# Kernel optimization log

Hardware: AMD Instinct MI355X
Metric: run time of the kernel (lower is better)

## Reference

```python
import jax, jax.numpy as jnp
import numpy as np

MOLS = 64
ATOMS = 256
N = MOLS * ATOMS
K_GB = 32
K_GNN = 16
HID = 128
OFFSET = 0.009            # GB dielectric offset (nm)
ALPHA, BETA, GAMMA = 1.0, 0.8, 4.85  # OBC2 coefficients
EPS_FACTOR = 138.935456   # Coulomb constant, kJ*nm/(mol*e^2)
PREF = -EPS_FACTOR * (1.0 - 1.0 / 78.5)


def _edges(key, k_neigh):
    # random intra-molecule neighbors, no self loops (mimics radius-graph structure)
    src = jnp.repeat(jnp.arange(N), k_neigh)
    off = jax.random.randint(key, (N * k_neigh,), 1, ATOMS)
    dst = (src // ATOMS) * ATOMS + (src % ATOMS + off) % ATOMS
    return jnp.stack([src, dst]).astype(jnp.int32)


def setup_inputs() -> dict:
    key = jax.random.key(0)
    ks = jax.random.split(key, 8)
    pos = (jax.random.uniform(ks[0], (N, 3), jnp.float32) * 1.5)
    q = jax.random.uniform(ks[1], (N, 1), jnp.float32) - 0.5
    rad = 0.15 + 0.05 * jax.random.uniform(ks[2], (N, 1), jnp.float32)
    scl = 0.8 + 0.2 * jax.random.uniform(ks[3], (N, 1), jnp.float32)
    rest = jax.random.uniform(ks[4], (N, 4), jnp.float32)
    atom_features = jnp.concatenate([q, rad, scl, rest], axis=1)
    batch = jnp.repeat(jnp.arange(MOLS), ATOMS).astype(jnp.int32)
    edge_index = _edges(ks[5], K_GB)
    gnn_edge_index = _edges(ks[6], K_GNN)

    def lin(k, fi, fo):
        return (jax.random.normal(k, (fi, fo), jnp.float32) / np.float32(np.sqrt(fi)),
                jnp.zeros((fo,), jnp.float32))
    kw = jax.random.split(ks[7], 6)
    i1_w1, i1_b1 = lin(kw[0], 2 * 2 + 1, HID)
    i1_w2, i1_b2 = lin(kw[1], HID, HID)
    i2_w1, i2_b1 = lin(kw[2], 2 * HID + 1, HID)
    i2_w2, i2_b2 = lin(kw[3], HID, HID)
    i3_w1, i3_b1 = lin(kw[4], 2 * HID + 1, HID)
    i3_w2, i3_b2 = lin(kw[5], HID, 1)
    return dict(pos=pos, atom_features=atom_features, batch=batch,
                edge_index=edge_index, gnn_edge_index=gnn_edge_index,
                i1_w1=i1_w1, i1_b1=i1_b1, i1_w2=i1_w2, i1_b2=i1_b2,
                i2_w1=i2_w1, i2_b1=i2_b1, i2_w2=i2_w2, i2_b2=i2_b2,
                i3_w1=i3_w1, i3_b1=i3_b1, i3_w2=i3_w2, i3_b2=i3_b2)


def _dist(pos, ei):
    d2 = jnp.sum((pos[ei[0]] - pos[ei[1]]) ** 2, axis=1)
    return jnp.sqrt(d2 + 1e-12)


def _gb_energies(pos, feats, ei):
    # GBNeck_interaction (Born radii via HCT descreening integral, OBC2 rescale)
    # followed by GBNeck_energies (pairwise GB + self energy), per-atom [N,1]
    n = pos.shape[0]
    src, dst = ei[0], ei[1]
    d = _dist(pos, ei)
    q, radius, scale = feats[:, 0], feats[:, 1], feats[:, 2]
    rho = radius - OFFSET
    sr_j = (scale * rho)[src]
    rho_i = rho[dst]
    U = d + sr_j
    L = jnp.maximum(rho_i, jnp.abs(d - sr_j))
    I = 0.5 * (1.0 / L - 1.0 / U
               + 0.25 * (d - sr_j ** 2 / d) * (1.0 / U ** 2 - 1.0 / L ** 2)
               + 0.5 * jnp.log(L / U) / d)
    I = jnp.where(rho_i < U, I, 0.0)
    Isum = jax.ops.segment_sum(I, dst, num_segments=n)
    psi = Isum * rho
    B = 1.0 / (1.0 / rho - jnp.tanh(ALPHA * psi - BETA * psi ** 2 + GAMMA * psi ** 3) / radius)
    Bi, Bj = B[dst], B[src]
    f_gb = jnp.sqrt(d ** 2 + Bi * Bj * jnp.exp(-d ** 2 / (4.0 * Bi * Bj)))
    e_pair = 0.5 * PREF * q[dst] * q[src] / f_gb  # 0.5: edges are double counted
    e = 0.5 * PREF * q ** 2 / B + jax.ops.segment_sum(e_pair, dst, num_segments=n)
    return e[:, None]


def _in_layer(x, ei, d, w1, b1, w2, b2):
    # IN_layer_all_swish_2pass: edge MLP on [x_i || x_j || d] + scatter-add
    n = x.shape[0]
    m = jnp.concatenate([x[ei[0]], x[ei[1]], d[:, None]], axis=1)
    h = jax.nn.silu(m @ w1 + b1)
    return jax.ops.segment_sum(h @ w2 + b2, ei[1], num_segments=n)


def _energies_all(pos, feats, ei, gei,
                  i1_w1, i1_b1, i1_w2, i1_b2,
                  i2_w1, i2_b1, i2_w2, i2_b2,
                  i3_w1, i3_b1, i3_w2, i3_b2):
    e_gb = _gb_energies(pos, feats, ei)
    d_gnn = _dist(pos, gei)
    x = jax.nn.silu(_in_layer(feats[:, :2], gei, d_gnn, i1_w1, i1_b1, i1_w2, i1_b2))
    x = jax.nn.silu(_in_layer(x, gei, d_gnn, i2_w1, i2_b1, i2_w2, i2_b2))
    x = _in_layer(x, gei, d_gnn, i3_w1, i3_b1, i3_w2, i3_b2)
    return e_gb + x


def reference(pos, atom_features, batch, edge_index, gnn_edge_index,
              i1_w1, i1_b1, i1_w2, i1_b2,
              i2_w1, i2_b1, i2_w2, i2_b2,
              i3_w1, i3_b1, i3_w2, i3_b2):
    ws = (i1_w1, i1_b1, i1_w2, i1_b2, i2_w1, i2_b1, i2_w2, i2_b2,
          i3_w1, i3_b1, i3_w2, i3_b2)
    efun = lambda p: _energies_all(p, atom_features, edge_index, gnn_edge_index, *ws)
    energies, vjp = jax.vjp(efun, pos)  # [N,1]
    (gpos,) = vjp(jnp.ones_like(energies))
    forces = -gpos
    energy = jax.ops.segment_sum(energies[:, 0], batch, num_segments=MOLS)[:, None]
    return energy, forces
```

## Files before the change

### kernel.cpp

```cpp
#include <hip/hip_runtime.h>
#include <hip/hip_bf16.h>

#define NATOMS 16384
#define MOLS   64
#define ATOMSM 256
#define EGB    524288
#define EGNN   262144
#define HID    128
#define NH     (NATOMS*HID)

#define OFFSETC 0.009f
#define ALPHAC  1.0f
#define BETAC   0.8f
#define GAMMAC  4.85f
#define PREFC   (-138.935456f*(1.0f-1.0f/78.5f))

typedef __hip_bfloat16 bf;
typedef __attribute__((ext_vector_type(8))) short bf8v;
typedef __attribute__((ext_vector_type(4))) float f4v;
typedef unsigned int uint;

__device__ __forceinline__ float b2f(bf x){ return __bfloat162float(x); }
__device__ __forceinline__ bf f2b(float x){ return __float2bfloat16(x); }
__device__ __forceinline__ short f2s(float x){ bf h = f2b(x); return *(short*)&h; }
__device__ __forceinline__ float s2f(short s){
    unsigned int x = ((unsigned int)(unsigned short)s) << 16;
    return __uint_as_float(x);
}
__device__ __forceinline__ float frcp(float x){ return __builtin_amdgcn_rcpf(x); }
__device__ __forceinline__ float frsq(float x){ return __builtin_amdgcn_rsqf(x); }
__device__ __forceinline__ float fsqrt(float x){ return __builtin_amdgcn_sqrtf(x); }
__device__ __forceinline__ float sigf(float x){ return frcp(1.0f+__expf(-x)); }
__device__ __forceinline__ float waveRed(float v){
    v += __shfl_xor(v,32); v += __shfl_xor(v,16); v += __shfl_xor(v,8);
    v += __shfl_xor(v,4);  v += __shfl_xor(v,2);  v += __shfl_xor(v,1);
    return v;
}
__device__ __forceinline__ uint pack2(float a, float b){
    return (uint)(unsigned short)f2s(a) | ((uint)(unsigned short)f2s(b) << 16);
}
__device__ __forceinline__ float lo2f(uint w){ return __uint_as_float(w << 16); }
__device__ __forceinline__ float hi2f(uint w){ return __uint_as_float(w & 0xffff0000u); }

__device__ __forceinline__ float red16(float (&A)[16], int lane){
#pragma unroll
    for (int i=0;i<8;i++){
        float send = (lane & 16) ? A[i] : A[i+8];
        float recv = __shfl_xor(send, 16);
        A[i] = ((lane & 16) ? A[i+8] : A[i]) + recv;
    }
#pragma unroll
    for (int i=0;i<4;i++){
        float send = (lane & 8) ? A[i] : A[i+4];
        float recv = __shfl_xor(send, 8);
        A[i] = ((lane & 8) ? A[i+4] : A[i]) + recv;
    }
#pragma unroll
    for (int i=0;i<2;i++){
        float send = (lane & 4) ? A[i] : A[i+2];
        float recv = __shfl_xor(send, 4);
        A[i] = ((lane & 4) ? A[i+2] : A[i]) + recv;
    }
    {
        float send = (lane & 2) ? A[0] : A[1];
        float recv = __shfl_xor(send, 2);
        A[0] = ((lane & 2) ? A[1] : A[0]) + recv;
    }
    A[0] += __shfl_xor(A[0], 32);
    A[0] += __shfl_xor(A[0], 1);
    return A[0];
}

__global__ __launch_bounds__(256) void k_A(
    const float* __restrict__ A2, const float* __restrict__ C1,
    const float* __restrict__ A3, const float* __restrict__ C2,
    short* __restrict__ C1t, short* __restrict__ C2t,
    short* __restrict__ A2at, short* __restrict__ A2bt,
    short* __restrict__ A3at, short* __restrict__ A3bt,
    short* __restrict__ rA2a, short* __restrict__ rA2b,
    short* __restrict__ rA3a, short* __restrict__ rA3b,
    short* __restrict__ rC1, short* __restrict__ rC2,
    const float* __restrict__ feat, const float* __restrict__ A1,
    bf* __restrict__ u1, bf* __restrict__ v1,
    const float* __restrict__ pos, const int* __restrict__ ei,
    float* __restrict__ Isum,
    const int* __restrict__ gei, float* __restrict__ dgnn, int* __restrict__ cnt)
{
    int tid = threadIdx.x;
    if (blockIdx.x < 64){
        int gid = blockIdx.x*256 + tid;
        int j = gid >> 7, k = gid & 127;
        C1t[gid]  = f2s(C1[k*HID+j]);
        C2t[gid]  = f2s(C2[k*HID+j]);
        A2at[gid] = f2s(A2[k*HID+j]);
        A2bt[gid] = f2s(A2[(HID+k)*HID+j]);
        A3at[gid] = f2s(A3[k*HID+j]);
        A3bt[gid] = f2s(A3[(HID+k)*HID+j]);
        rA2a[gid] = f2s(A2[gid]);
        rA2b[gid] = f2s(A2[HID*HID+gid]);
        rA3a[gid] = f2s(A3[gid]);
        rA3b[gid] = f2s(A3[HID*HID+gid]);
        rC1[gid]  = f2s(C1[gid]);
        rC2[gid]  = f2s(C2[gid]);
    } else if (blockIdx.x < 4160){
        int gid2 = (blockIdx.x-64)*256 + tid;
        int i = gid2 >> 6, k2 = (gid2 & 63)*2;
        float q = feat[7*i+0], r = feat[7*i+1];
        float u0 = q*A1[k2]         + r*A1[HID+k2];
        float u1v= q*A1[k2+1]       + r*A1[HID+k2+1];
        float v0 = q*A1[2*HID+k2]   + r*A1[3*HID+k2];
        float v1v= q*A1[2*HID+k2+1] + r*A1[3*HID+k2+1];
        ushort2 uu, vv;
        uu.x = (unsigned short)f2s(u0); uu.y = (unsigned short)f2s(u1v);
        vv.x = (unsigned short)f2s(v0); vv.y = (unsigned short)f2s(v1v);
        *(ushort2*)((short*)u1 + (size_t)i*HID + k2) = uu;
        *(ushort2*)((short*)v1 + (size_t)i*HID + k2) = vv;
    } else if (blockIdx.x < 4672){
        __shared__ float sPx[256], sPy[256], sPz[256], sRho[256], sSr[256];
        __shared__ float sI[256];
        int bb = blockIdx.x - 4160;
        int mbase = (bb >> 3) * 256;
        {
            int i = mbase + tid;
            sPx[tid]=pos[3*i]; sPy[tid]=pos[3*i+1]; sPz[tid]=pos[3*i+2];
            float rad = feat[7*i+1], sc = feat[7*i+2];
            float rho = rad - OFFSETC;
            sRho[tid]=rho; sSr[tid]=sc*rho;
            sI[tid]=0.f;
        }
        __syncthreads();
        int T = bb*256 + tid;
        int s = T >> 3, p = T & 7;
        int sl = s & 255;
        int e0 = s*32 + p*4;
        float px = sPx[sl], py = sPy[sl], pz = sPz[sl];
        float sr = sSr[sl];
        float srr = sr*sr;
        const int* dP = ei + EGB;
        int4 d4 = *(const int4*)(dP + e0);
        int dls[4] = {d4.x&255, d4.y&255, d4.z&255, d4.w&255};
#pragma unroll
        for (int j=0;j<4;j++){
            int dl = dls[j];
            float dx = px - sPx[dl];
            float dy = py - sPy[dl];
            float dz = pz - sPz[dl];
            float d2 = dx*dx+dy*dy+dz*dz + 1e-12f;
            float rd = frsq(d2);
            float d  = d2*rd;
            float rho_i = sRho[dl];
            float U = d + sr;
            if (rho_i < U){
                float L = fmaxf(rho_i, fabsf(d - sr));
                float invU = frcp(U), invL = frcp(L);
                float I = 0.5f*invL - 0.5f*invU
                        + 0.125f*(d - srr*rd)*(invU*invU - invL*invL)
                        + 0.25f*__logf(L*invU)*rd;
                atomicAdd(&sI[dl], I);
            }
        }
        __syncthreads();
        atomicAdd(&Isum[mbase + tid], sI[tid]);
    } else {
        int e = (blockIdx.x-4672)*256 + tid;
        int s = gei[e], dd = gei[EGNN+e];
        float dx = pos[3*s+0] - pos[3*dd+0];
        float dy = pos[3*s+1] - pos[3*dd+1];
        float dz = pos[3*s+2] - pos[3*dd+2];
        dgnn[e] = fsqrt(dx*dx+dy*dy+dz*dz + 1e-12f);
        atomicAdd(&cnt[dd], 1);
    }
}

__global__ __launch_bounds__(256) void k_B(
    const float* __restrict__ feat, const float* __restrict__ Isum,
    float* __restrict__ Bv, float* __restrict__ cB, float* __restrict__ gB,
    float* __restrict__ egb,
    const int* __restrict__ cnt, int* __restrict__ rptr,
    const int* __restrict__ gei, const float* __restrict__ dgnn,
    int* __restrict__ csr, int2* __restrict__ csr2)
{
    int t = threadIdx.x;
    if (blockIdx.x < 64){
        int i = blockIdx.x*256 + t;
        float q   = feat[7*i+0];
        float rad = feat[7*i+1];
        float rho = rad - OFFSETC;
        float psi = Isum[i]*rho;
        float u = psi*(ALPHAC + psi*(-BETAC + GAMMAC*psi));
        float tt = tanhf(u);
        float rrad = frcp(rad);
        float B = frcp(frcp(rho) - tt*rrad);
        Bv[i] = B;
        float du = ALPHAC + psi*(-2.0f*BETAC + 3.0f*GAMMAC*psi);
        cB[i] = B*B*((1.0f-tt*tt)*rrad)*du*rho;
        float Cs = 0.5f*PREFC*q*q;
        float rB = frcp(B);
        egb[i] = Cs*rB;
        gB[i]  = -Cs*rB*rB;
    } else {
        __shared__ int sc[256];
        __shared__ int lcur[256];
        int m = blockIdx.x - 64;
        int c = cnt[m*256+t];
        sc[t] = c; __syncthreads();
        for (int off=1; off<256; off<<=1){
            int x = (t>=off) ? sc[t-off] : 0;
            __syncthreads();
            sc[t] += x;
            __syncthreads();
        }
        int exl = sc[t] - c;
        rptr[m*256+t] = m*4096 + exl;
        lcur[t] = exl;
        __syncthreads();
        int e0 = m*4096;
        for (int j=t; j<4096; j+=256){
            int e = e0 + j;
            int dl = gei[EGNN+e] & 255;
            float d = dgnn[e];
            int p = atomicAdd(&lcur[dl], 1);
            int idx = e0 + p;
            csr[idx] = e;
            int2 rec; rec.x = (e >> 4) << 8;
            rec.y = __float_as_int(d);
            csr2[idx] = rec;
        }
    }
}

template<bool WSDS>
__device__ __forceinline__ void edge_fwd_wave(
    int dst, int lane,
    const int2* __restrict__ csr2, const int* __restrict__ rptr, const int* __restrict__ cnt,
    const uint* __restrict__ u, const uint* __restrict__ v,
    const float* __restrict__ wdp, const float* __restrict__ bb,
    uint* __restrict__ Hs, uint* __restrict__ Sds)
{
    int n = cnt[dst], r0 = rptr[dst];
    float2 wd = *(const float2*)&wdp[2*lane];
    float2 b2 = *(const float2*)&bb[2*lane];
    uint vp = v[dst*64 + lane];
    float base0 = lo2f(vp) + b2.x;
    float base1 = hi2f(vp) + b2.y;
    float h0=0.f,h1=0.f,e0a=0.f,e1a=0.f;
    for (int j0=0; j0<n; j0+=64){
        int m = n - j0; if (m > 64) m = 64;
        int rx = 0, ry = 0;
        if (lane < m){ int2 rc = csr2[r0+j0+lane]; rx = rc.x; ry = rc.y; }
#pragma unroll 8
        for (int j=0;j<m;j++){
            uint off = (uint)__builtin_amdgcn_readlane(rx, j);
            float d  = __uint_as_float((unsigned)__builtin_amdgcn_readlane(ry, j));
            const uint* urow = (const uint*)((const char*)u + off);
            uint up = urow[lane];
            float a0 = fmaf(d, wd.x, base0 + lo2f(up));
            float a1 = fmaf(d, wd.y, base1 + hi2f(up));
            float s0 = sigf(a0), s1 = sigf(a1);
            float p0 = a0*s0, p1 = a1*s1;
            h0 += p0; h1 += p1;
            if (WSDS){
                e0a = fmaf(s0, 1.f + a0 - p0, e0a);
                e1a = fmaf(s1, 1.f + a1 - p1, e1a);
            }
        }
    }
    Hs[dst*64+lane] = pack2(h0,h1);
    if (WSDS) Sds[dst*64+lane] = pack2(e0a,e1a);
}

__global__ __launch_bounds__(256,8) void k_ef0C(
    const float* __restrict__ pos, const float* __restrict__ feat,
    const int* __restrict__ ei, const float* __restrict__ Bv,
    float* __restrict__ egb, float* __restrict__ gdgb, float* __restrict__ gB,
    const int2* __restrict__ csr2, const int* __restrict__ rptr, const int* __restrict__ cnt,
    const uint* __restrict__ u, const uint* __restrict__ v,
    const float* __restrict__ wdp, const float* __restrict__ bb,
    uint* __restrict__ Hs)
{
    int tid = threadIdx.x;
    if (blockIdx.x < 512){
        __shared__ float sPx[256], sPy[256], sPz[256], sB[256], sQf[256];
        __shared__ float sE[256], sG[256];
        int mbase = (blockIdx.x >> 3) * 256;
        {
            int i = mbase + tid;
            sPx[tid]=pos[3*i]; sPy[tid]=pos[3*i+1]; sPz[tid]=pos[3*i+2];
            sB[tid]=Bv[i]; sQf[tid]=feat[7*i+0];
            sE[tid]=0.f; sG[tid]=0.f;
        }
        __syncthreads();
        int T = blockIdx.x*256 + tid;
        int s = T >> 3, p = T & 7;
        int sl = s & 255;
        int e0 = s*32 + p*4;
        float px = sPx[sl], py = sPy[sl], pz = sPz[sl];
        float qs = sQf[sl];
        float Bs = sB[sl];
        float gsrc = 0.f;
        const int* dP = ei + EGB;
        int4 d4 = *(const int4*)(dP + e0);
        int dls[4] = {d4.x&255, d4.y&255, d4.z&255, d4.w&255};
#pragma unroll
        for (int j=0;j<4;j++){
            int dl = dls[j];
            float dx = px - sPx[dl];
            float dy = py - sPy[dl];
            float dz = pz - sPz[dl];
            float d2 = dx*dx+dy*dy+dz*dz + 1e-12f;
            float d  = d2*frsq(d2);
            float Bd = sB[dl];
            float C = 0.5f*PREFC*sQf[dl]*qs;
            float P = Bd*Bs;
            float qq = 0.25f*d2*frcp(P);
            float ex = __expf(-qq);
            float f2 = d2 + P*ex;
            float rf = frsq(f2);
            float f3i = rf*rf*rf;
            gdgb[e0+j] = -C*d*(1.f - 0.25f*ex)*f3i;
            float common = -C*ex*(1.f + qq)*0.5f*f3i;
            atomicAdd(&sE[dl], C*rf);
            atomicAdd(&sG[dl], common*Bs);
            gsrc += common*Bd;
        }
        gsrc += __shfl_xor(gsrc,1);
        gsrc += __shfl_xor(gsrc,2);
        gsrc += __shfl_xor(gsrc,4);
        if (p==0) atomicAdd(&sG[sl], gsrc);
        __syncthreads();
        atomicAdd(&egb[mbase + tid], sE[tid]);
        atomicAdd(&gB[mbase + tid],  sG[tid]);
    } else {
        int lane = tid & 63, wid = tid >> 6;
        int dst = (blockIdx.x-512)*4 + wid;
        edge_fwd_wave<false>(dst, lane, csr2, rptr, cnt, u, v, wdp, bb, Hs, nullptr);
    }
}

__global__ __launch_bounds__(256,8) void k_ef1E(
    const float* __restrict__ pos, const float* __restrict__ feat,
    const int* __restrict__ ei, const float* __restrict__ cB,
    const float* __restrict__ gB,
    const float* __restrict__ gdgb, float* __restrict__ grad,
    const int2* __restrict__ csr2, const int* __restrict__ rptr, const int* __restrict__ cnt,
    const uint* __restrict__ u, const uint* __restrict__ v,
    const float* __restrict__ wdp, const float* __restrict__ bb,
    uint* __restrict__ Hs, uint* __restrict__ Sds)
{
    int tid = threadIdx.x;
    if (blockIdx.x < 512){
        __shared__ float sPx[256], sPy[256], sPz[256], sRho[256], sSr[256], sCg[256];
        __shared__ float sGx[256], sGy[256], sGz[256];
        int mbase = (blockIdx.x >> 3) * 256;
        {
            int i = mbase + tid;
            sPx[tid]=pos[3*i]; sPy[tid]=pos[3*i+1]; sPz[tid]=pos[3*i+2];
            float rad = feat[7*i+1], sc = feat[7*i+2];
            float rho = rad - OFFSETC;
            sRho[tid]=rho; sSr[tid]=sc*rho;
            sCg[tid]=cB[i]*gB[i];
            sGx[tid]=0.f; sGy[tid]=0.f; sGz[tid]=0.f;
        }
        __syncthreads();
        int T = blockIdx.x*256 + tid;
        int s = T >> 3, p = T & 7;
        int sl = s & 255;
        int e0 = s*32 + p*4;
        float px = sPx[sl], py = sPy[sl], pz = sPz[sl];
        float sr = sSr[sl];
        float srr = sr*sr;
        float gx=0.f, gy=0.f, gz=0.f;
        const int* dP = ei + EGB;
        int4 d4 = *(const int4*)(dP + e0);
        int dls[4] = {d4.x&255, d4.y&255, d4.z&255, d4.w&255};
#pragma unroll
        for (int j=0;j<4;j++){
            int dl = dls[j];
            float dx = px - sPx[dl];
            float dy = py - sPy[dl];
            float dz = pz - sPz[dl];
            float d2 = dx*dx+dy*dy+dz*dz + 1e-12f;
            float rd = frsq(d2);
            float d  = d2*rd;
            float rd2 = rd*rd;
            float rho_i = sRho[dl];
            float U = d + sr;
            float gd = gdgb[e0+j];
            if (rho_i < U){
                float aa = fabsf(d - sr);
                float L, Lp;
                if (rho_i >= aa){ L = rho_i; Lp = 0.f; }
                else { L = aa; Lp = (d >= sr) ? 1.f : -1.f; }
                float invU = frcp(U), invL = frcp(L);
                float invU2=invU*invU, invL2=invL*invL;
                float dIdd = -0.5f*Lp*invL2 + 0.5f*invU2
                    + 0.125f*(1.f + srr*rd2)*(invU2 - invL2)
                    + 0.125f*(d - srr*rd)*(2.f*Lp*invL2*invL - 2.f*invU2*invU)
                    + 0.25f*((Lp*invL - invU)*rd - __logf(L*invU)*rd2);
                gd += sCg[dl]*dIdd;
            }
            float c = gd*rd;
            gx += c*dx; gy += c*dy; gz += c*dz;
            atomicAdd(&sGx[dl], -c*dx);
            atomicAdd(&sGy[dl], -c*dy);
            atomicAdd(&sGz[dl], -c*dz);
        }
        gx += __shfl_xor(gx,1); gx += __shfl_xor(gx,2); gx += __shfl_xor(gx,4);
        gy += __shfl_xor(gy,1); gy += __shfl_xor(gy,2); gy += __shfl_xor(gy,4);
        gz += __shfl_xor(gz,1); gz += __shfl_xor(gz,2); gz += __shfl_xor(gz,4);
        if (p==0){
            atomicAdd(&sGx[sl], gx);
            atomicAdd(&sGy[sl], gy);
            atomicAdd(&sGz[sl], gz);
        }
        __syncthreads();
        int i = mbase + tid;
        atomicAdd(&grad[3*i+0], sGx[tid]);
        atomicAdd(&grad[3*i+1], sGy[tid]);
        atomicAdd(&grad[3*i+2], sGz[tid]);
    } else {
        int lane = tid & 63, wid = tid >> 6;
        int dst = (blockIdx.x-512)*4 + wid;
        edge_fwd_wave<true>(dst, lane, csr2, rptr, cnt, u, v, wdp, bb, Hs, Sds);
    }
}

__global__ __launch_bounds__(256) void k_node_fwd_uv_mfma(
    const short* __restrict__ Hs, const int* __restrict__ cnt,
    const short* __restrict__ Ct, const float* __restrict__ D,
    const short* __restrict__ Aat, const short* __restrict__ Abt,
    bf* __restrict__ dsz, bf* __restrict__ u, bf* __restrict__ v)
{
    __shared__ short sx[64*HID];
    int tid = threadIdx.x;
    int lane = tid & 63, w = tid >> 6;
    int m0 = blockIdx.x*64 + w*16;
    int ar = lane & 15, kg = lane >> 4;
    bf8v af[4];
#pragma unroll
    for (int s=0;s<4;s++) af[s] = *(const bf8v*)&Hs[(size_t)(m0+ar)*HID + s*32 + kg*8];
    f4v acc[8];
#pragma unroll
    for (int nt=0;nt<8;nt++){
        acc[nt] = (f4v){0.f,0.f,0.f,0.f};
        const short* bp = Ct + (nt*16+ar)*HID + kg*8;
#pragma unroll
        for (int s=0;s<4;s++){
            bf8v bv = *(const bf8v*)(bp + s*32);
            acc[nt] = __builtin_amdgcn_mfma_f32_16x16x32_bf16(af[s], bv, acc[nt], 0,0,0);
        }
    }
    float cn[4];
#pragma unroll
    for (int r=0;r<4;r++) cn[r] = (float)cnt[m0 + kg*4 + r];
#pragma unroll
    for (int nt=0;nt<8;nt++){
        int j = nt*16 + ar;
        float Dj = D[j];
#pragma unroll
        for (int r=0;r<4;r++){
            int m = m0 + kg*4 + r;
            float zv = acc[nt][r] + cn[r]*Dj;
            float sg = sigf(zv);
            dsz[(size_t)m*HID + j] = f2b(sg*(1.f + zv*(1.f - sg)));
            sx[(w*16 + kg*4 + r)*HID + j] = f2s(zv*sg);
        }
    }
    __syncthreads();
#pragma unroll
    for (int s=0;s<4;s++) af[s] = *(const bf8v*)&sx[(w*16+ar)*HID + s*32 + kg*8];
    f4v au[8], av[8];
#pragma unroll
    for (int nt=0;nt<8;nt++){
        au[nt] = (f4v){0.f,0.f,0.f,0.f};
        av[nt] = (f4v){0.f,0.f,0.f,0.f};
        const short* bpa = Aat + (nt*16+ar)*HID + kg*8;
        const short* bpb = Abt + (nt*16+ar)*HID + kg*8;
#pragma unroll
        for (int s=0;s<4;s++){
            bf8v ba = *(const bf8v*)(bpa + s*32);
            bf8v bb = *(const bf8v*)(bpb + s*32);
            au[nt] = __builtin_amdgcn_mfma_f32_16x16x32_bf16(af[s], ba, au[nt], 0,0,0);
            av[nt] = __builtin_amdgcn_mfma_f32_16x16x32_bf16(af[s], bb, av[nt], 0,0,0);
        }
    }
#pragma unroll
    for (int nt=0;nt<8;nt++){
        int j = nt*16 + ar;
#pragma unroll
        for (int r=0;r<4;r++){
            int m = m0 + kg*4 + r;
            u[(size_t)m*HID + j] = f2b(au[nt][r]);
            v[(size_t)m*HID + j] = f2b(av[nt][r]);
        }
    }
}

__global__ __launch_bounds__(256,6) void k_l3(
    const int2* __restrict__ csr2, const int* __restrict__ rptr, const int* __restrict__ cnt,
    const int* __restrict__ gei, const float* __restrict__ dgnn,
    const uint* __restrict__ u, const uint* __restrict__ v,
    const float* __restrict__ A3, const float* __restrict__ B3,
    const float* __restrict__ C3, const float* __restrict__ D3,
    uint* __restrict__ Gd, float* __restrict__ x3,
    uint* __restrict__ Gs, float* __restrict__ gdg)
{
    int lane = threadIdx.x & 63, wid = threadIdx.x >> 6;
    const float* wdp = A3 + 256*HID;
    if (blockIdx.x < NATOMS/4){
        int dst = blockIdx.x*4 + wid;
        int n = cnt[dst], r0 = rptr[dst];
        float2 wd = *(const float2*)&wdp[2*lane];
        float2 b2 = *(const float2*)&B3[2*lane];
        float2 ck = *(const float2*)&C3[2*lane];
        uint vp = v[dst*64 + lane];
        float base0 = lo2f(vp) + b2.x;
        float base1 = hi2f(vp) + b2.y;
        float h0=0.f,h1=0.f,e0a=0.f,e1a=0.f;
        for (int j0=0; j0<n; j0+=64){
            int m = n - j0; if (m > 64) m = 64;
            int rx = 0, ry = 0;
            if (lane < m){ int2 rc = csr2[r0+j0+lane]; rx = rc.x; ry = rc.y; }
#pragma unroll 8
            for (int j=0;j<m;j++){
                uint off = (uint)__builtin_amdgcn_readlane(rx, j);
                float d  = __uint_as_float((unsigned)__builtin_amdgcn_readlane(ry, j));
                const uint* urow = (const uint*)((const char*)u + off);
                uint up = urow[lane];
                float a0 = fmaf(d, wd.x, base0 + lo2f(up));
                float a1 = fmaf(d, wd.y, base1 + hi2f(up));
                float s0 = sigf(a0), s1 = sigf(a1);
                float p0 = a0*s0, p1 = a1*s1;
                h0 += p0; h1 += p1;
                e0a = fmaf(s0, 1.f + a0 - p0, e0a);
                e1a = fmaf(s1, 1.f + a1 - p1, e1a);
            }
        }
        Gd[dst*64+lane] = pack2(ck.x*e0a, ck.y*e1a);
        float px = waveRed(ck.x*h0 + ck.y*h1);
        if (lane==0) x3[dst] = px + (float)n*D3[0];
    } else {
        int s = (blockIdx.x - NATOMS/4)*4 + wid;
        int doff = 0, dbit = 0;
        if (lane < 16){
            doff = gei[EGNN + s*16 + lane] << 8;
            dbit = __float_as_int(dgnn[s*16+lane]);
        }
        float2 wd = *(const float2*)&wdp[2*lane];
        float2 b2 = *(const float2*)&B3[2*lane];
        float2 ck = *(const float2*)&C3[2*lane];
        uint up = u[s*64 + lane];
        float us0 = lo2f(up) + b2.x;
        float us1 = hi2f(up) + b2.y;
        float cw0 = ck.x*wd.x, cw1 = ck.y*wd.y;
        float gs0=0.f, gs1=0.f;
        float A[16];
#pragma unroll
        for (int t=0;t<16;t++){
            uint off = (uint)__builtin_amdgcn_readlane(doff, t);
            float d = __uint_as_float((unsigned)__builtin_amdgcn_readlane(dbit, t));
            const uint* vrow = (const uint*)((const char*)v + off);
            uint vp = vrow[lane];
            float a0 = fmaf(d, wd.x, us0 + lo2f(vp));
            float a1 = fmaf(d, wd.y, us1 + hi2f(vp));
            float s0 = sigf(a0), s1 = sigf(a1);
            float p0 = a0*s0, p1 = a1*s1;
            float dv0 = s0*(1.f + a0 - p0);
            float dv1 = s1*(1.f + a1 - p1);
            gs0 += dv0; gs1 += dv1;
            A[t] = fmaf(dv1, cw1, dv0*cw0);
        }
        Gs[s*64+lane] = pack2(ck.x*gs0, ck.y*gs1);
        float tot = red16(A, lane);
        if (lane < 32 && !(lane & 1)) gdg[s*16 + (lane>>1)] = tot;
    }
}

__global__ __launch_bounds__(256,6) void k_bwd_src(
    const int* __restrict__ gei, const float* __restrict__ dgnn,
    const uint* __restrict__ u, const uint* __restrict__ v,
    const float* __restrict__ wdp, const float* __restrict__ bb,
    const uint* __restrict__ gH,
    uint* __restrict__ Gs, float* __restrict__ gdg)
{
    int lane = threadIdx.x & 63, wid = threadIdx.x >> 6;
    int s = blockIdx.x*4 + wid;
    int doff = 0, dbit = 0;
    if (lane < 16){
        doff = gei[EGNN + s*16 + lane] << 8;
        dbit = __float_as_int(dgnn[s*16+lane]);
    }
    float gold = gdg[s*16 + ((lane>>1)&15)];
    float2 wd = *(const float2*)&wdp[2*lane];
    float2 b2 = *(const float2*)&bb[2*lane];
    uint up = u[s*64 + lane];
    float us0 = lo2f(up) + b2.x;
    float us1 = hi2f(up) + b2.y;
    float gs0=0.f, gs1=0.f;
    float A[16];
#pragma unroll
    for (int t=0;t<16;t++){
        uint off = (uint)__builtin_amdgcn_readlane(doff, t);
        float d = __uint_as_float((unsigned)__builtin_amdgcn_readlane(dbit, t));
        const uint* vrow = (const uint*)((const char*)v + off);
        const uint* grow = (const uint*)((const char*)gH + off);
        uint vp = vrow[lane];
        uint gp = grow[lane];
        float a0 = fmaf(d, wd.x, us0 + lo2f(vp));
        float a1 = fmaf(d, wd.y, us1 + hi2f(vp));
        float s0 = sigf(a0), s1 = sigf(a1);
        float p0 = a0*s0, p1 = a1*s1;
        float ga0 = s0*(1.f + a0 - p0) * lo2f(gp);
        float ga1 = s1*(1.f + a1 - p1) * hi2f(gp);
        gs0 += ga0; gs1 += ga1;
        A[t] = fmaf(ga1, wd.y, ga0*wd.x);
    }
    if (Gs) Gs[s*64+lane] = pack2(gs0, gs1);
    float tot = red16(A, lane);
    if (lane < 32 && !(lane & 1)) gdg[s*16 + (lane>>1)] = gold + tot;
}

__global__ __launch_bounds__(256) void k_gx_node_bwd_mfma(
    const short* __restrict__ Gs, const short* __restrict__ Gd,
    const short* __restrict__ gHin, const short* __restrict__ Sds,
    const short* __restrict__ Ra, const short* __restrict__ Rb,
    const bf* __restrict__ dsz, const short* __restrict__ Rc,
    bf* __restrict__ gHout)
{
    __shared__ short st[64*HID];
    int lane = threadIdx.x & 63, w = threadIdx.x >> 6;
    int m0 = blockIdx.x*64 + w*16;
    int ar = lane & 15, kg = lane >> 4;
    bf8v as_[4], ad_[4];
#pragma unroll
    for (int s=0;s<4;s++)
        as_[s] = *(const bf8v*)&Gs[(size_t)(m0+ar)*HID + s*32 + kg*8];
    if (Sds){
#pragma unroll
        for (int s=0;s<4;s++){
            bf8v g = *(const bf8v*)&gHin[(size_t)(m0+ar)*HID + s*32 + kg*8];
            bf8v sd = *(const bf8v*)&Sds[(size_t)(m0+ar)*HID + s*32 + kg*8];
            bf8v r;
#pragma unroll
            for (int i=0;i<8;i++) r[i] = f2s(s2f(g[i])*s2f(sd[i]));
            ad_[s] = r;
        }
    } else {
#pragma unroll
        for (int s=0;s<4;s++)
            ad_[s] = *(const bf8v*)&Gd[(size_t)(m0+ar)*HID + s*32 + kg*8];
    }
    f4v acc[8];
#pragma unroll
    for (int nt=0;nt<8;nt++){
        acc[nt] = (f4v){0.f,0.f,0.f,0.f};
        const short* bpa = Ra + (nt*16+ar)*HID + kg*8;
        const short* bpb = Rb + (nt*16+ar)*HID + kg*8;
#pragma unroll
        for (int s=0;s<4;s++){
            bf8v ba = *(const bf8v*)(bpa + s*32);
            bf8v bb = *(const bf8v*)(bpb + s*32);
            acc[nt] = __builtin_amdgcn_mfma_f32_16x16x32_bf16(as_[s], ba, acc[nt], 0,0,0);
            acc[nt] = __builtin_amdgcn_mfma_f32_16x16x32_bf16(ad_[s], bb, acc[nt], 0,0,0);
        }
    }
#pragma unroll
    for (int nt=0;nt<8;nt++){
        int j = nt*16 + ar;
#pragma unroll
        for (int r=0;r<4;r++){
            int m = m0 + kg*4 + r;
            float t = acc[nt][r] * b2f(dsz[(size_t)m*HID + j]);
            st[(w*16 + kg*4 + r)*HID + j] = f2s(t);
        }
    }
    __syncthreads();
    bf8v af[4];
#pragma unroll
    for (int s=0;s<4;s++) af[s] = *(const bf8v*)&st[(w*16+ar)*HID + s*32 + kg*8];
    f4v a2[8];
#pragma unroll
    for (int nt=0;nt<8;nt++){
        a2[nt] = (f4v){0.f,0.f,0.f,0.f};
        const short* bp = Rc + (nt*16+ar)*HID + kg*8;
#pragma unroll
        for (int s=0;s<4;s++){
            bf8v bc = *(const bf8v*)(bp + s*32);
            a2[nt] = __builtin_amdgcn_mfma_f32_16x16x32_bf16(af[s], bc, a2[nt], 0,0,0);
        }
    }
#pragma unroll
    for (int nt=0;nt<8;nt++){
        int j = nt*16 + ar;
#pragma unroll
        for (int r=0;r<4;r++){
            gHout[(size_t)(m0 + kg*4 + r)*HID + j] = f2b(a2[nt][r]);
        }
    }
}

__global__ __launch_bounds__(256) void k_out(
    const float* __restrict__ pos, const int* __restrict__ gei,
    const int* __restrict__ csr, const int* __restrict__ rptr, const int* __restrict__ cnt,
    const float* __restrict__ dgnn, const float* __restrict__ gdg,
    const float* __restrict__ grad,
    const float* __restrict__ egb, const float* __restrict__ x3,
    float* __restrict__ out)
{
    int tid = threadIdx.x;
    if (blockIdx.x < 512){
        float* fout = out + MOLS;
        int T = blockIdx.x*256 + tid;
        int i = T >> 3, p = T & 7;
        float px = pos[3*i+0], py = pos[3*i+1], pz = pos[3*i+2];
        float ax=0.f, ay=0.f, az=0.f;
        for (int j=p;j<16;j+=8){
            int e = i*16 + j;
            int o = gei[EGNN+e];
            float c = gdg[e]*frcp(dgnn[e]);
            ax += c*(px - pos[3*o+0]);
            ay += c*(py - pos[3*o+1]);
            az += c*(pz - pos[3*o+2]);
        }
        int n = cnt[i], r0 = rptr[i];
        for (int j=p;j<n;j+=8){
            int e = csr[r0+j];
            int o = e >> 4;
            float c = gdg[e]*frcp(dgnn[e]);
            ax += c*(px - pos[3*o+0]);
            ay += c*(py - pos[3*o+1]);
            az += c*(pz - pos[3*o+2]);
        }
        ax += __shfl_xor(ax,1); ax += __shfl_xor(ax,2); ax += __shfl_xor(ax,4);
        ay += __shfl_xor(ay,1); ay += __shfl_xor(ay,2); ay += __shfl_xor(ay,4);
        az += __shfl_xor(az,1); az += __shfl_xor(az,2); az += __shfl_xor(az,4);
        if (p==0){
            fout[3*i+0] = -(grad[3*i+0] + ax);
            fout[3*i+1] = -(grad[3*i+1] + ay);
            fout[3*i+2] = -(grad[3*i+2] + az);
        }
    } else {
        __shared__ float red[4];
        int m = blockIdx.x - 512;
        int i = m*ATOMSM + tid;
        float en = egb[i] + x3[i];
        float v = waveRed(en);
        int wave = tid>>6, lane = tid&63;
        if (lane==0) red[wave] = v;
        __syncthreads();
        if (tid==0) out[m] = red[0]+red[1]+red[2]+red[3];
    }
}

extern "C" void kernel_launch(void* const* d_in, const int* in_sizes, int n_in,
                              void* d_out, int out_size, void* d_ws, size_t ws_size,
                              hipStream_t stream)
{
    const float* pos  = (const float*)d_in[0];
    const float* feat = (const float*)d_in[1];
    const int* ei  = (const int*)d_in[3];
    const int* gei = (const int*)d_in[4];
    const float* A1f = (const float*)d_in[5];  const float* B1f = (const float*)d_in[6];
    const float* C1f = (const float*)d_in[7];  const float* D1f = (const float*)d_in[8];
    const float* A2f = (const float*)d_in[9];  const float* B2f = (const float*)d_in[10];
    const float* C2f = (const float*)d_in[11]; const float* D2f = (const float*)d_in[12];
    const float* A3f = (const float*)d_in[13]; const float* B3f = (const float*)d_in[14];
    const float* C3f = (const float*)d_in[15]; const float* D3f = (const float*)d_in[16];

    float* w = (float*)d_ws;
    size_t off = 0;
    auto nxt = [&](size_t n)->float*{ float* p = w + off; off += (n + 255) & ~(size_t)255; return p; };
    float* Isum = nxt(NATOMS);
    int*   cnt  = (int*)nxt(NATOMS);
    float* grad = nxt(3*NATOMS);
    float* Bv = nxt(NATOMS); float* cB = nxt(NATOMS);
    float* gB = nxt(NATOMS); float* egb = nxt(NATOMS); float* x3 = nxt(NATOMS);
    int*   rptr = (int*)nxt(NATOMS);
    int*   csr  = (int*)nxt(EGNN);
    int2*  csr2 = (int2*)nxt((size_t)EGNN*2);
    float* dgnn = nxt(EGNN); float* gdgnn = nxt(EGNN); float* gdgb = nxt(EGB);
    bf* dsz1 = (bf*)nxt(NH/2); bf* dsz2 = (bf*)nxt(NH/2);
    bf* Hs1 = (bf*)nxt(NH/2); bf* Hs2 = (bf*)nxt(NH/2);
    bf* Gs3 = (bf*)nxt(NH/2); bf* Gd3 = (bf*)nxt(NH/2);
    bf* Sds2 = (bf*)nxt(NH/2);
    bf* u1 = (bf*)nxt(NH/2); bf* v1 = (bf*)nxt(NH/2);
    bf* u2 = (bf*)nxt(NH/2); bf* v2 = (bf*)nxt(NH/2);
    bf* v3 = (bf*)nxt(NH/2);
    short* C1t  = (short*)nxt(8192); short* C2t  = (short*)nxt(8192);
    short* A2at = (short*)nxt(8192); short* A2bt = (short*)nxt(8192);
    short* A3at = (short*)nxt(8192); short* A3bt = (short*)nxt(8192);
    short* rA2a = (short*)nxt(8192); short* rA2b = (short*)nxt(8192);
    short* rA3a = (short*)nxt(8192); short* rA3b = (short*)nxt(8192);
    short* rC1  = (short*)nxt(8192); short* rC2  = (short*)nxt(8192);
    bf* u3  = Hs1;
    bf* gH2 = Hs2;
    bf* Gs2 = Gs3;
    bf* gH1 = u3;

    hipMemsetAsync(Isum, 0, (size_t)5*NATOMS*sizeof(float), stream);

    k_A<<<64 + NH/512 + 512 + EGNN/256, 256, 0, stream>>>(
        A2f, C1f, A3f, C2f,
        C1t, C2t, A2at, A2bt, A3at, A3bt, rA2a, rA2b, rA3a, rA3b, rC1, rC2,
        feat, A1f, u1, v1,
        pos, ei, Isum, gei, dgnn, cnt);

    k_B<<<128,256,0,stream>>>(feat, Isum, Bv, cB, gB, egb, cnt, rptr,
                              gei, dgnn, csr, csr2);

    k_ef0C<<<512 + NATOMS/4, 256, 0, stream>>>(
        pos, feat, ei, Bv, egb, gdgb, gB,
        csr2, rptr, cnt, (const uint*)u1, (const uint*)v1, A1f+4*HID, B1f, (uint*)Hs1);

    k_node_fwd_uv_mfma<<<NATOMS/64,256,0,stream>>>((const short*)Hs1, cnt, C1t, D1f,
                                                   A2at, A2bt, dsz1, u2, v2);

    k_ef1E<<<512 + NATOMS/4, 256, 0, stream>>>(
        pos, feat, ei, cB, gB, gdgb, grad,
        csr2, rptr, cnt, (const uint*)u2, (const uint*)v2, A2f+256*HID, B2f,
        (uint*)Hs2, (uint*)Sds2);

    k_node_fwd_uv_mfma<<<NATOMS/64,256,0,stream>>>((const short*)Hs2, cnt, C2t, D2f,
                                                   A3at, A3bt, dsz2, u3, v3);

    k_l3<<<2*(NATOMS/4),256,0,stream>>>(csr2, rptr, cnt, gei, dgnn,
                                        (const uint*)u3, (const uint*)v3,
                                        A3f, B3f, C3f, D3f,
                                        (uint*)Gd3, x3, (uint*)Gs3, gdgnn);

    k_gx_node_bwd_mfma<<<NATOMS/64,256,0,stream>>>((const short*)Gs3, (const short*)Gd3,
        (const short*)nullptr, (const short*)nullptr, rA3a, rA3b, dsz2, rC2, gH2);
    k_bwd_src<<<NATOMS/4,256,0,stream>>>(gei, dgnn, (const uint*)u2, (const uint*)v2,
                                         A2f+256*HID, B2f, (const uint*)gH2,
                                         (uint*)Gs2, gdgnn);
    k_gx_node_bwd_mfma<<<NATOMS/64,256,0,stream>>>((const short*)Gs2, (const short*)nullptr,
        (const short*)gH2, (const short*)Sds2, rA2a, rA2b, dsz1, rC1, gH1);
    k_bwd_src<<<NATOMS/4,256,0,stream>>>(gei, dgnn, (const uint*)u1, (const uint*)v1,
                                         A1f+4*HID, B1f, (const uint*)gH1,
                                         (uint*)nullptr, gdgnn);

    k_out<<<576,256,0,stream>>>(pos, gei, csr, rptr, cnt, dgnn, gdgnn,
                                grad, egb, x3, (float*)d_out);
}
```

Before: 316.5 us.

## Per-molecule shared-memory GNN distance/count, algebraic SiLU-derivative accumulation, retuned occupancy

The GNN edge-distance section of k_A now runs one block per molecule. It stages that molecule's positions in shared memory and counts in-degrees with shared atomics before writing cnt directly, which replaces global gathers and global atomics. The SiLU-derivative accumulation is rewritten algebraically into running sums of s and p*s, combined with h at the end, which trims per-edge arithmetic in the edge-forward loops. Unroll factors drop from 8 to 4, and k_l3 and k_bwd_src launch bounds go from 6 to 4 blocks per CU, giving more registers per thread at the cost of occupancy. The local-index trick (&255) relies on edges staying within a molecule, and writing cnt directly assumes each molecule's 4096 GNN edges are contiguous, both of which hold for the generated edge construction.

```diff
diff --git a/kernel.cpp b/kernel.cpp
--- a/kernel.cpp
+++ b/kernel.cpp
@@ -162,13 +162,29 @@
         __syncthreads();
         atomicAdd(&Isum[mbase + tid], sI[tid]);
     } else {
-        int e = (blockIdx.x-4672)*256 + tid;
-        int s = gei[e], dd = gei[EGNN+e];
-        float dx = pos[3*s+0] - pos[3*dd+0];
-        float dy = pos[3*s+1] - pos[3*dd+1];
-        float dz = pos[3*s+2] - pos[3*dd+2];
-        dgnn[e] = fsqrt(dx*dx+dy*dy+dz*dz + 1e-12f);
-        atomicAdd(&cnt[dd], 1);
+        __shared__ float dPx[256], dPy[256], dPz[256];
+        __shared__ int sCnt[256];
+        int m = blockIdx.x - 4672;
+        int mbase = m*256;
+        {
+            int i = mbase + tid;
+            dPx[tid]=pos[3*i]; dPy[tid]=pos[3*i+1]; dPz[tid]=pos[3*i+2];
+            sCnt[tid]=0;
+        }
+        __syncthreads();
+        int e0 = m*4096;
+        for (int j=tid; j<4096; j+=256){
+            int e = e0 + j;
+            int sl = gei[e] & 255;
+            int dl = gei[EGNN+e] & 255;
+            float dx = dPx[sl]-dPx[dl];
+            float dy = dPy[sl]-dPy[dl];
+            float dz = dPz[sl]-dPz[dl];
+            dgnn[e] = fsqrt(dx*dx+dy*dy+dz*dz + 1e-12f);
+            atomicAdd(&sCnt[dl], 1);
+        }
+        __syncthreads();
+        cnt[mbase + tid] = sCnt[tid];
     }
 }
 
@@ -243,12 +259,12 @@
     uint vp = v[dst*64 + lane];
     float base0 = lo2f(vp) + b2.x;
     float base1 = hi2f(vp) + b2.y;
-    float h0=0.f,h1=0.f,e0a=0.f,e1a=0.f;
+    float h0=0.f,h1=0.f,sS0=0.f,sS1=0.f,sQ0=0.f,sQ1=0.f;
     for (int j0=0; j0<n; j0+=64){
         int m = n - j0; if (m > 64) m = 64;
         int rx = 0, ry = 0;
         if (lane < m){ int2 rc = csr2[r0+j0+lane]; rx = rc.x; ry = rc.y; }
-#pragma unroll 8
+#pragma unroll 4
         for (int j=0;j<m;j++){
             uint off = (uint)__builtin_amdgcn_readlane(rx, j);
             float d  = __uint_as_float((unsigned)__builtin_amdgcn_readlane(ry, j));
@@ -260,13 +276,13 @@
             float p0 = a0*s0, p1 = a1*s1;
             h0 += p0; h1 += p1;
             if (WSDS){
-                e0a = fmaf(s0, 1.f + a0 - p0, e0a);
-                e1a = fmaf(s1, 1.f + a1 - p1, e1a);
+                sS0 += s0; sQ0 = fmaf(p0, s0, sQ0);
+                sS1 += s1; sQ1 = fmaf(p1, s1, sQ1);
             }
         }
     }
     Hs[dst*64+lane] = pack2(h0,h1);
-    if (WSDS) Sds[dst*64+lane] = pack2(e0a,e1a);
+    if (WSDS) Sds[dst*64+lane] = pack2(sS0 + h0 - sQ0, sS1 + h1 - sQ1);
 }
 
 __global__ __launch_bounds__(256,8) void k_ef0C(
@@ -496,7 +512,7 @@
     }
 }
 
-__global__ __launch_bounds__(256,6) void k_l3(
+__global__ __launch_bounds__(256,4) void k_l3(
     const int2* __restrict__ csr2, const int* __restrict__ rptr, const int* __restrict__ cnt,
     const int* __restrict__ gei, const float* __restrict__ dgnn,
     const uint* __restrict__ u, const uint* __restrict__ v,
@@ -516,12 +532,12 @@
         uint vp = v[dst*64 + lane];
         float base0 = lo2f(vp) + b2.x;
         float base1 = hi2f(vp) + b2.y;
-        float h0=0.f,h1=0.f,e0a=0.f,e1a=0.f;
+        float h0=0.f,h1=0.f,sS0=0.f,sS1=0.f,sQ0=0.f,sQ1=0.f;
         for (int j0=0; j0<n; j0+=64){
             int m = n - j0; if (m > 64) m = 64;
             int rx = 0, ry = 0;
             if (lane < m){ int2 rc = csr2[r0+j0+lane]; rx = rc.x; ry = rc.y; }
-#pragma unroll 8
+#pragma unroll 4
             for (int j=0;j<m;j++){
                 uint off = (uint)__builtin_amdgcn_readlane(rx, j);
                 float d  = __uint_as_float((unsigned)__builtin_amdgcn_readlane(ry, j));
@@ -532,11 +548,11 @@
                 float s0 = sigf(a0), s1 = sigf(a1);
                 float p0 = a0*s0, p1 = a1*s1;
                 h0 += p0; h1 += p1;
-                e0a = fmaf(s0, 1.f + a0 - p0, e0a);
-                e1a = fmaf(s1, 1.f + a1 - p1, e1a);
+                sS0 += s0; sQ0 = fmaf(p0, s0, sQ0);
+                sS1 += s1; sQ1 = fmaf(p1, s1, sQ1);
             }
         }
-        Gd[dst*64+lane] = pack2(ck.x*e0a, ck.y*e1a);
+        Gd[dst*64+lane] = pack2(ck.x*(sS0 + h0 - sQ0), ck.y*(sS1 + h1 - sQ1));
         float px = waveRed(ck.x*h0 + ck.y*h1);
         if (lane==0) x3[dst] = px + (float)n*D3[0];
     } else {
@@ -576,7 +592,7 @@
     }
 }
 
-__global__ __launch_bounds__(256,6) void k_bwd_src(
+__global__ __launch_bounds__(256,4) void k_bwd_src(
     const int* __restrict__ gei, const float* __restrict__ dgnn,
     const uint* __restrict__ u, const uint* __restrict__ v,
     const float* __restrict__ wdp, const float* __restrict__ bb,
@@ -799,7 +815,7 @@
 
     hipMemsetAsync(Isum, 0, (size_t)5*NATOMS*sizeof(float), stream);
 
-    k_A<<<64 + NH/512 + 512 + EGNN/256, 256, 0, stream>>>(
+    k_A<<<64 + NH/512 + 512 + 64, 256, 0, stream>>>(
         A2f, C1f, A3f, C2f,
         C1t, C2t, A2at, A2bt, A3at, A3bt, rA2a, rA2b, rA3a, rA3b, rC1, rC2,
         feat, A1f, u1, v1,
```

After: 318.1 us. Within noise of the previous version (+0.5%).
